# Kernel tuning notes

Hardware: AMD Instinct MI355X
Metric: run time of the kernel (lower is better)

Reference implementation:

```python
import jax, jax.numpy as jnp
import numpy as np


def setup_inputs() -> dict:
    key = jax.random.key(0)
    k1, k2, k3, k4 = jax.random.split(key, 4)
    B, n, f, k = 32768, 512, 30, 40
    X = jax.random.normal(k1, (B, n), dtype=jnp.float32)
    w1 = jax.random.normal(k2, (n, 1), dtype=jnp.float32) * 0.01
    b = jnp.zeros((1,), dtype=jnp.float32)
    v = jax.random.normal(k3, (n, f, k), dtype=jnp.float32) * 0.01
    feature2field = jax.random.randint(k4, (n,), 0, f, dtype=jnp.int32)
    return {"X": X, "w1": w1, "b": b, "v": v, "feature2field": feature2field}


def reference(X, w1, b, v, feature2field):
    # linear terms: [B]
    linear = (X @ w1).reshape(-1) + b[0]
    n = v.shape[0]
    # A[i, j] = v[i, feature2field[j]]  -> [n, n, k]
    A = v[:, feature2field, :]
    # pair coefficient C[i, j] = sum_k v[i, field[j], k] * v[j, field[i], k]
    C = jnp.einsum('ijk,jik->ij', A, A)
    # strict upper triangle matches the i<j loop in the original
    Cm = C * jnp.triu(jnp.ones((n, n), dtype=C.dtype), k=1)
    # interaction[b] = sum_{i<j} C[i,j] * X[b,i] * X[b,j]
    inter = jnp.einsum('bi,ij,bj->b', X, Cm, X)
    logits = linear + inter
    return jax.nn.sigmoid(logits)
```

## Files before the change

### kernel.cpp

```cpp
#include <hip/hip_runtime.h>
#include <hip/hip_bf16.h>
#include <math.h>


#define N_FEAT 512
#define FK 1200
#define KDIM 40
#define B_ROWS 32768
#define BM 64
#define BK2 128

typedef __attribute__((ext_vector_type(8))) short short8;
typedef __attribute__((ext_vector_type(4))) float f32x4;

__device__ __forceinline__ unsigned short bf16_rne(float f) {
    union { float f; unsigned int u; } c; c.f = f;
    unsigned int u = c.u;
    u += 0x7fffu + ((u >> 16) & 1u);
    return (unsigned short)(u >> 16);
}

__device__ __forceinline__ float bf16_to_f(unsigned short h) {
    union { unsigned int u; float f; } c;
    c.u = ((unsigned int)h) << 16;
    return c.f;
}

__device__ __forceinline__ void async_copy16(const void* g, void* l) {
    __builtin_amdgcn_global_load_lds(
        (const __attribute__((address_space(1))) void*)g,
        (__attribute__((address_space(3))) void*)l,
        16, 0, 0);
}

#define FENCE() asm volatile("" ::: "memory")

__global__ __launch_bounds__(256) void build_w16(const float* __restrict__ v,
                                                 const int* __restrict__ f2f,
                                                 unsigned short* __restrict__ W16) {
    __shared__ float a_lds[FK];
    __shared__ float c_lds[256 * 44];

    const int i   = blockIdx.y;
    const int j0  = blockIdx.x * 256;
    const int tid = threadIdx.x;
    const int fi  = f2f[i];

    for (int q = tid; q < FK; q += 256) a_lds[q] = v[(size_t)i * FK + q];
    for (int q = tid; q < 2560; q += 256) {
        const int jl = q / 10, c4 = q % 10;
        *(float4*)&c_lds[jl * 44 + c4 * 4] =
            *(const float4*)&v[(size_t)(j0 + jl) * FK + fi * KDIM + c4 * 4];
    }
    __syncthreads();

    const int j  = j0 + tid;
    const int fj = f2f[j];
    const float4* a = (const float4*)&a_lds[fj * KDIM];
    const float4* c = (const float4*)&c_lds[tid * 44];
    float acc = 0.f;
#pragma unroll
    for (int q = 0; q < KDIM / 4; ++q) {
        float4 av = a[q], cv = c[q];
        acc = fmaf(av.x, cv.x, acc);
        acc = fmaf(av.y, cv.y, acc);
        acc = fmaf(av.z, cv.z, acc);
        acc = fmaf(av.w, cv.w, acc);
    }
    W16[(size_t)i * N_FEAT + j] = (i == j) ? (unsigned short)0 : bf16_rne(0.5f * acc);
}

__global__ __launch_bounds__(512, 2) void ffm_fused(const float* __restrict__ X,
                                                    const unsigned short* __restrict__ W16,
                                                    const float* __restrict__ w1,
                                                    const float* __restrict__ bvec,
                                                    float* __restrict__ out) {
    __shared__ __align__(16) unsigned short As[BM * N_FEAT];
    __shared__ __align__(16) unsigned short Bs[2][128 * BK2];
    __shared__ float part[4 * BM];

    const int tid  = threadIdx.x;
    const int lane = tid & 63;
    const int wave = tid >> 6;
    const int wm = wave & 1;
    const int wn = wave >> 1;
    const int quad = lane >> 4;
    const int l16  = lane & 15;
    const int aswz = l16 & 7;

    const size_t row0 = (size_t)blockIdx.x * BM;

    float w1v[4][2];
#pragma unroll
    for (int cb = 0; cb < 4; ++cb)
#pragma unroll
        for (int ni = 0; ni < 2; ++ni)
            w1v[cb][ni] = w1[cb * 128 + wn * 32 + ni * 16 + l16];
    const float bias = bvec[0];

    auto stage = [&](int s) {
        const int col0 = (s >> 2) * 128;
        const int k0   = (s & 3) * BK2;
        unsigned short* dst = (unsigned short*)Bs[s & 1];
#pragma unroll
        for (int i = 0; i < 4; ++i) {
            const int r = wave * 16 + i * 4 + quad;
            async_copy16(W16 + (size_t)(col0 + r) * N_FEAT + k0 + ((l16 ^ (r & 7)) << 3),
                         dst + r * BK2 + l16 * 8);
        }
    };

    stage(0);
    {
        const float4* X4 = (const float4*)(X + row0 * N_FEAT);
#pragma unroll
        for (int u = 0; u < 8; ++u) {
            const int g  = u * 512 + tid;
            const int r  = g >> 6;
            const int cc = g & 63;
            float4 f0 = X4[r * 128 + cc * 2];
            float4 f1 = X4[r * 128 + cc * 2 + 1];
            union { unsigned short us[8]; short8 v; } pk;
            pk.us[0] = bf16_rne(f0.x);
            pk.us[1] = bf16_rne(f0.y);
            pk.us[2] = bf16_rne(f0.z);
            pk.us[3] = bf16_rne(f0.w);
            pk.us[4] = bf16_rne(f1.x);
            pk.us[5] = bf16_rne(f1.y);
            pk.us[6] = bf16_rne(f1.z);
            pk.us[7] = bf16_rne(f1.w);
            *(short8*)(As + r * N_FEAT + ((cc ^ (r & 7)) << 3)) = pk.v;
        }
    }
    asm volatile("s_waitcnt lgkmcnt(0)" ::: "memory");
    __builtin_amdgcn_s_barrier();
    FENCE();

    short8 areg[2][16];
#pragma unroll
    for (int ka = 0; ka < 16; ++ka)
#pragma unroll
        for (int mi = 0; mi < 2; ++mi) {
            const int ar = wm * 32 + mi * 16 + l16;
            areg[mi][ka] = *(const short8*)(As + ar * N_FEAT + (((ka * 4 + quad) ^ aswz) << 3));
        }

    float rs[2][4];
#pragma unroll
    for (int mi = 0; mi < 2; ++mi)
#pragma unroll
        for (int reg = 0; reg < 4; ++reg) rs[mi][reg] = 0.f;

    f32x4 acc[2][2];
#pragma unroll
    for (int mi = 0; mi < 2; ++mi)
#pragma unroll
        for (int ni = 0; ni < 2; ++ni)
            acc[mi][ni] = (f32x4){0.f, 0.f, 0.f, 0.f};

#pragma unroll
    for (int cb = 0; cb < 4; ++cb) {
        const int col0 = cb * 128;
#pragma unroll
        for (int t = 0; t < 4; ++t) {
            const int s = cb * 4 + t;
            if (s < 15) {
                stage(s + 1);
                asm volatile("s_waitcnt vmcnt(4)" ::: "memory");
            } else {
                asm volatile("s_waitcnt vmcnt(0)" ::: "memory");
            }
            __builtin_amdgcn_s_barrier();
            FENCE();

            const unsigned short* bs = (const unsigned short*)Bs[s & 1];
            __builtin_amdgcn_s_setprio(1);
#pragma unroll
            for (int kk = 0; kk < 4; ++kk) {
                const int ka = t * 4 + kk;
                short8 b[2];
                const int swc = ((kk * 4 + quad) ^ aswz) << 3;
#pragma unroll
                for (int ni = 0; ni < 2; ++ni) {
                    const int br = wn * 32 + ni * 16 + l16;
                    b[ni] = *(const short8*)(bs + br * BK2 + swc);
                }
#pragma unroll
                for (int mi = 0; mi < 2; ++mi)
#pragma unroll
                    for (int ni = 0; ni < 2; ++ni)
                        acc[mi][ni] = __builtin_amdgcn_mfma_f32_16x16x32_bf16(
                            areg[mi][ka], b[ni], acc[mi][ni], 0, 0, 0);
            }
            __builtin_amdgcn_s_setprio(0);

            FENCE();
            __builtin_amdgcn_s_barrier();
            FENCE();
        }

#pragma unroll
        for (int mi = 0; mi < 2; ++mi) {
#pragma unroll
            for (int ni = 0; ni < 2; ++ni) {
                const int gc = col0 + wn * 32 + ni * 16 + l16;
#pragma unroll
                for (int reg = 0; reg < 4; ++reg) {
                    const int row = wm * 32 + mi * 16 + quad * 4 + reg;
                    const int adr = row * N_FEAT + ((((gc >> 3) ^ (row & 7)) << 3) | (gc & 7));
                    const float xf = bf16_to_f(As[adr]);
                    rs[mi][reg] = fmaf(xf, acc[mi][ni][reg] + w1v[cb][ni], rs[mi][reg]);
                }
                acc[mi][ni] = (f32x4){0.f, 0.f, 0.f, 0.f};
            }
        }
    }

#pragma unroll
    for (int mi = 0; mi < 2; ++mi)
#pragma unroll
        for (int reg = 0; reg < 4; ++reg) {
            float r = rs[mi][reg];
#pragma unroll
            for (int off = 1; off < 16; off <<= 1)
                r += __shfl_xor(r, off, 16);
            if (l16 == 0)
                part[wn * BM + wm * 32 + mi * 16 + quad * 4 + reg] = r;
        }
    __syncthreads();

    if (tid < BM) {
        const float t = part[tid] + part[BM + tid] + part[2 * BM + tid] +
                        part[3 * BM + tid] + bias;
        out[row0 + tid] = 1.0f / (1.0f + expf(-t));
    }
}

extern "C" void kernel_launch(void* const* d_in, const int* in_sizes, int n_in,
                              void* d_out, int out_size, void* d_ws, size_t ws_size,
                              hipStream_t stream) {
    const float* X   = (const float*)d_in[0];
    const float* w1  = (const float*)d_in[1];
    const float* b   = (const float*)d_in[2];
    const float* v   = (const float*)d_in[3];
    const int*   f2f = (const int*)d_in[4];
    float* out = (float*)d_out;

    unsigned short* W16 = (unsigned short*)d_ws;

    build_w16<<<dim3(2, N_FEAT), 256, 0, stream>>>(v, f2f, W16);
    ffm_fused<<<B_ROWS / BM, 512, 0, stream>>>(X, W16, w1, b, out);
}
```

Measured before the change: 155.2 us.

## Restructure fused FFM GEMM to 32x32 MFMA with full-width output per wave

Each wave now owns 64 of the 512 output columns for all 64 rows and accumulates across the full K in 32x32x16 MFMA registers. The A tile is stored k-major in LDS instead of being preloaded into registers, and W is streamed in K slices of 32 for all columns. The epilogue reads X directly from global memory in fp32 rather than the bf16 LDS copy, and the cross-wave reduction widens to 8 partials. The aim is to remove the per-column-block epilogue and register-resident A, and to use the larger MFMA shape. In exchange LDS use grows and occupancy drops to one block per CU.

```diff
diff --git a/kernel.cpp b/kernel.cpp
--- a/kernel.cpp
+++ b/kernel.cpp
@@ -8,22 +8,17 @@
 #define KDIM 40
 #define B_ROWS 32768
 #define BM 64
-#define BK2 128
+#define BKS 32
+#define NSTEP 16
 
 typedef __attribute__((ext_vector_type(8))) short short8;
-typedef __attribute__((ext_vector_type(4))) float f32x4;
+typedef __attribute__((ext_vector_type(16))) float f32x16;
 
 __device__ __forceinline__ unsigned short bf16_rne(float f) {
     union { float f; unsigned int u; } c; c.f = f;
     unsigned int u = c.u;
     u += 0x7fffu + ((u >> 16) & 1u);
     return (unsigned short)(u >> 16);
-}
-
-__device__ __forceinline__ float bf16_to_f(unsigned short h) {
-    union { unsigned int u; float f; } c;
-    c.u = ((unsigned int)h) << 16;
-    return c.f;
 }
 
 __device__ __forceinline__ void async_copy16(const void* g, void* l) {
@@ -70,44 +65,30 @@
     W16[(size_t)i * N_FEAT + j] = (i == j) ? (unsigned short)0 : bf16_rne(0.5f * acc);
 }
 
-__global__ __launch_bounds__(512, 2) void ffm_fused(const float* __restrict__ X,
+__global__ __launch_bounds__(512, 1) void ffm_fused(const float* __restrict__ X,
                                                     const unsigned short* __restrict__ W16,
                                                     const float* __restrict__ w1,
                                                     const float* __restrict__ bvec,
                                                     float* __restrict__ out) {
     __shared__ __align__(16) unsigned short As[BM * N_FEAT];
-    __shared__ __align__(16) unsigned short Bs[2][128 * BK2];
-    __shared__ float part[4 * BM];
+    __shared__ __align__(16) unsigned short Bs[2][N_FEAT * BKS];
+    __shared__ float part[8 * BM];
 
     const int tid  = threadIdx.x;
     const int lane = tid & 63;
     const int wave = tid >> 6;
-    const int wm = wave & 1;
-    const int wn = wave >> 1;
-    const int quad = lane >> 4;
-    const int l16  = lane & 15;
-    const int aswz = l16 & 7;
+    const int half = lane >> 5;
+    const int l31  = lane & 31;
 
     const size_t row0 = (size_t)blockIdx.x * BM;
 
-    float w1v[4][2];
-#pragma unroll
-    for (int cb = 0; cb < 4; ++cb)
-#pragma unroll
-        for (int ni = 0; ni < 2; ++ni)
-            w1v[cb][ni] = w1[cb * 128 + wn * 32 + ni * 16 + l16];
-    const float bias = bvec[0];
+    const unsigned short* wrow = W16 + (size_t)(wave * 64 + lane) * N_FEAT;
 
     auto stage = [&](int s) {
-        const int col0 = (s >> 2) * 128;
-        const int k0   = (s & 3) * BK2;
         unsigned short* dst = (unsigned short*)Bs[s & 1];
 #pragma unroll
-        for (int i = 0; i < 4; ++i) {
-            const int r = wave * 16 + i * 4 + quad;
-            async_copy16(W16 + (size_t)(col0 + r) * N_FEAT + k0 + ((l16 ^ (r & 7)) << 3),
-                         dst + r * BK2 + l16 * 8);
-        }
+        for (int i = 0; i < 4; ++i)
+            async_copy16(wrow + s * BKS + i * 8, dst + (i * 512 + wave * 64) * 8);
     };
 
     stage(0);
@@ -117,9 +98,9 @@
         for (int u = 0; u < 8; ++u) {
             const int g  = u * 512 + tid;
             const int r  = g >> 6;
-            const int cc = g & 63;
-            float4 f0 = X4[r * 128 + cc * 2];
-            float4 f1 = X4[r * 128 + cc * 2 + 1];
+            const int kc = g & 63;
+            float4 f0 = X4[r * 128 + kc * 2];
+            float4 f1 = X4[r * 128 + kc * 2 + 1];
             union { unsigned short us[8]; short8 v; } pk;
             pk.us[0] = bf16_rne(f0.x);
             pk.us[1] = bf16_rne(f0.y);
@@ -129,110 +110,110 @@
             pk.us[5] = bf16_rne(f1.y);
             pk.us[6] = bf16_rne(f1.z);
             pk.us[7] = bf16_rne(f1.w);
-            *(short8*)(As + r * N_FEAT + ((cc ^ (r & 7)) << 3)) = pk.v;
+            *(short8*)(As + ((size_t)kc * 64 + (r ^ (kc & 7))) * 8) = pk.v;
         }
     }
     asm volatile("s_waitcnt lgkmcnt(0)" ::: "memory");
     __builtin_amdgcn_s_barrier();
     FENCE();
 
-    short8 areg[2][16];
-#pragma unroll
-    for (int ka = 0; ka < 16; ++ka)
-#pragma unroll
-        for (int mi = 0; mi < 2; ++mi) {
-            const int ar = wm * 32 + mi * 16 + l16;
-            areg[mi][ka] = *(const short8*)(As + ar * N_FEAT + (((ka * 4 + quad) ^ aswz) << 3));
-        }
-
-    float rs[2][4];
+    f32x16 acc[2][2];
 #pragma unroll
     for (int mi = 0; mi < 2; ++mi)
 #pragma unroll
-        for (int reg = 0; reg < 4; ++reg) rs[mi][reg] = 0.f;
-
-    f32x4 acc[2][2];
+        for (int ci = 0; ci < 2; ++ci)
+#pragma unroll
+            for (int r = 0; r < 16; ++r) acc[mi][ci][r] = 0.f;
+
+#pragma unroll
+    for (int t = 0; t < NSTEP; ++t) {
+        if (t < NSTEP - 1) {
+            stage(t + 1);
+            asm volatile("s_waitcnt vmcnt(4)" ::: "memory");
+        } else {
+            asm volatile("s_waitcnt vmcnt(0)" ::: "memory");
+        }
+        __builtin_amdgcn_s_barrier();
+        FENCE();
+
+        const unsigned short* bs = (const unsigned short*)Bs[t & 1];
+        __builtin_amdgcn_s_setprio(1);
+#pragma unroll
+        for (int si = 0; si < 2; ++si) {
+            const int kcg = t * 4 + si * 2 + half;
+            const int ksw = kcg & 7;
+            short8 a[2], b[2];
+#pragma unroll
+            for (int mi = 0; mi < 2; ++mi) {
+                const int ar = mi * 32 + l31;
+                a[mi] = *(const short8*)(As + ((size_t)kcg * 64 + (ar ^ ksw)) * 8);
+            }
+#pragma unroll
+            for (int ci = 0; ci < 2; ++ci) {
+                const int col = wave * 64 + ci * 32 + l31;
+                b[ci] = *(const short8*)(bs + ((size_t)(si * 2 + half) * 512 + col) * 8);
+            }
+#pragma unroll
+            for (int mi = 0; mi < 2; ++mi)
+#pragma unroll
+                for (int ci = 0; ci < 2; ++ci)
+                    acc[mi][ci] = __builtin_amdgcn_mfma_f32_32x32x16_bf16(
+                        a[mi], b[ci], acc[mi][ci], 0, 0, 0);
+        }
+        __builtin_amdgcn_s_setprio(0);
+        FENCE();
+        __builtin_amdgcn_s_barrier();
+        FENCE();
+    }
+
+    float w1v[2];
+#pragma unroll
+    for (int ci = 0; ci < 2; ++ci) w1v[ci] = w1[wave * 64 + ci * 32 + l31];
+    const float bias = bvec[0];
+
+    float rs[2][16];
+#pragma unroll
+    for (int mi = 0; mi < 2; ++mi) {
+#pragma unroll
+        for (int reg = 0; reg < 16; ++reg) {
+            const int row = mi * 32 + (reg & 3) + 8 * (reg >> 2) + 4 * half;
+            const float* xr = X + (row0 + row) * N_FEAT;
+            float s = 0.f;
+#pragma unroll
+            for (int ci = 0; ci < 2; ++ci) {
+                const int col = wave * 64 + ci * 32 + l31;
+                s = fmaf(xr[col], acc[mi][ci][reg] + w1v[ci], s);
+            }
+            rs[mi][reg] = s;
+        }
+    }
+
 #pragma unroll
     for (int mi = 0; mi < 2; ++mi)
 #pragma unroll
-        for (int ni = 0; ni < 2; ++ni)
-            acc[mi][ni] = (f32x4){0.f, 0.f, 0.f, 0.f};
-
-#pragma unroll
-    for (int cb = 0; cb < 4; ++cb) {
-        const int col0 = cb * 128;
-#pragma unroll
-        for (int t = 0; t < 4; ++t) {
-            const int s = cb * 4 + t;
-            if (s < 15) {
-                stage(s + 1);
-                asm volatile("s_waitcnt vmcnt(4)" ::: "memory");
-            } else {
-                asm volatile("s_waitcnt vmcnt(0)" ::: "memory");
-            }
-            __builtin_amdgcn_s_barrier();
-            FENCE();
-
-            const unsigned short* bs = (const unsigned short*)Bs[s & 1];
-            __builtin_amdgcn_s_setprio(1);
-#pragma unroll
-            for (int kk = 0; kk < 4; ++kk) {
-                const int ka = t * 4 + kk;
-                short8 b[2];
-                const int swc = ((kk * 4 + quad) ^ aswz) << 3;
-#pragma unroll
-                for (int ni = 0; ni < 2; ++ni) {
-                    const int br = wn * 32 + ni * 16 + l16;
-                    b[ni] = *(const short8*)(bs + br * BK2 + swc);
-                }
-#pragma unroll
-                for (int mi = 0; mi < 2; ++mi)
-#pragma unroll
-                    for (int ni = 0; ni < 2; ++ni)
-                        acc[mi][ni] = __builtin_amdgcn_mfma_f32_16x16x32_bf16(
-                            areg[mi][ka], b[ni], acc[mi][ni], 0, 0, 0);
-            }
-            __builtin_amdgcn_s_setprio(0);
-
-            FENCE();
-            __builtin_amdgcn_s_barrier();
-            FENCE();
-        }
-
-#pragma unroll
-        for (int mi = 0; mi < 2; ++mi) {
-#pragma unroll
-            for (int ni = 0; ni < 2; ++ni) {
-                const int gc = col0 + wn * 32 + ni * 16 + l16;
-#pragma unroll
-                for (int reg = 0; reg < 4; ++reg) {
-                    const int row = wm * 32 + mi * 16 + quad * 4 + reg;
-                    const int adr = row * N_FEAT + ((((gc >> 3) ^ (row & 7)) << 3) | (gc & 7));
-                    const float xf = bf16_to_f(As[adr]);
-                    rs[mi][reg] = fmaf(xf, acc[mi][ni][reg] + w1v[cb][ni], rs[mi][reg]);
-                }
-                acc[mi][ni] = (f32x4){0.f, 0.f, 0.f, 0.f};
-            }
-        }
-    }
-
-#pragma unroll
-    for (int mi = 0; mi < 2; ++mi)
-#pragma unroll
-        for (int reg = 0; reg < 4; ++reg) {
+        for (int reg = 0; reg < 16; ++reg) {
             float r = rs[mi][reg];
 #pragma unroll
-            for (int off = 1; off < 16; off <<= 1)
-                r += __shfl_xor(r, off, 16);
-            if (l16 == 0)
-                part[wn * BM + wm * 32 + mi * 16 + quad * 4 + reg] = r;
-        }
+            for (int off = 1; off < 32; off <<= 1)
+                r += __shfl_xor(r, off, 32);
+            rs[mi][reg] = r;
+        }
+    if (l31 == 0) {
+#pragma unroll
+        for (int mi = 0; mi < 2; ++mi)
+#pragma unroll
+            for (int reg = 0; reg < 16; ++reg) {
+                const int row = mi * 32 + (reg & 3) + 8 * (reg >> 2) + 4 * half;
+                part[wave * 64 + row] = rs[mi][reg];
+            }
+    }
     __syncthreads();
 
     if (tid < BM) {
-        const float t = part[tid] + part[BM + tid] + part[2 * BM + tid] +
-                        part[3 * BM + tid] + bias;
-        out[row0 + tid] = 1.0f / (1.0f + expf(-t));
+        float tsum = bias;
+#pragma unroll
+        for (int w = 0; w < 8; ++w) tsum += part[w * 64 + tid];
+        out[row0 + tid] = 1.0f / (1.0f + expf(-tsum));
     }
 }
 
```

Result: slower. 166.6 us (+7.4%).
